# Performance work log

Measured on AMD Instinct MI355X. Metric: run time of the kernel, lower is better.

The kernel has to match this reference:

```python
import jax, jax.numpy as jnp
import numpy as np

DK, DL, HID = 128, 128, 128  # per init_kwargs: mlp_list=[256,128,128]


def setup_inputs() -> dict:
    key = jax.random.key(0)
    k1, k2, k3, k4, k5 = jax.random.split(key, 5)
    B, K, L = 2, 128, 4096
    inputA = jax.random.normal(k1, (B, K, DK), dtype=jnp.float32)
    inputB = jax.random.normal(k2, (B, L, DL), dtype=jnp.float32)
    # MLP layer 0: Linear(256 -> 128), kaiming-uniform-ish init
    lim1 = 1.0 / np.sqrt(DK + DL)
    W1 = jax.random.uniform(k3, (DK + DL, HID), jnp.float32, -lim1, lim1)
    b1 = jax.random.uniform(k4, (HID,), jnp.float32, -lim1, lim1)
    # scoring Linear(128 -> 1, bias=False)
    lim2 = 1.0 / np.sqrt(HID)
    w2 = jax.random.uniform(k5, (HID,), jnp.float32, -lim2, lim2)
    return {"inputA": inputA, "inputB": inputB, "W1": W1, "b1": b1,
            "w2": w2, "nA": K, "nB": L}


def reference(inputA, inputB, W1, b1, w2, nA, nB):
    # Original: tC = cat([repeat(A), repeat(B)], -1); mlp(tC); linear; softmax(L).
    # Fused-equivalent math: split W1 rows between the A-part and B-part of the
    # concat, so the first Linear is two small matmuls + broadcast add.
    hA = jnp.einsum('bkd,dh->bkh', inputA, W1[:DK])        # (B, K, H)
    hB = jnp.einsum('bld,dh->blh', inputB, W1[DK:])        # (B, L, H)
    h = jax.nn.relu(hA[:, :, None, :] + hB[:, None, :, :] + b1)  # (B, K, L, H)
    scores = jnp.einsum('bklh,h->bkl', h, w2)              # (B, K, L)
    return jax.nn.softmax(scores, axis=2)
```

## Files before the change

### kernel.cpp

```cpp
#include <hip/hip_runtime.h>
#include <hip/hip_fp16.h>
#include <math.h>

constexpr int BB = 2;
constexpr int KK = 128;
constexpr int LL = 4096;
constexpr int DD = 128;
constexpr int HH = 128;

__device__ __forceinline__ float4 ld4(const float* p) {
    return *reinterpret_cast<const float4*>(p);
}

__device__ __forceinline__ __half2 hmax2(__half2 a, __half2 b) {
    unsigned ua = __builtin_bit_cast(unsigned, a);
    unsigned ub = __builtin_bit_cast(unsigned, b);
    unsigned ud;
    asm("v_pk_max_f16 %0, %1, %2" : "=v"(ud) : "v"(ua), "v"(ub));
    return __builtin_bit_cast(__half2, ud);
}

__global__ __launch_bounds__(256) void k1_gemm(
    const float* __restrict__ inA, const float* __restrict__ inB,
    const float* __restrict__ W1, const float* __restrict__ b1,
    __half* __restrict__ uh, __half* __restrict__ vh)
{
    __shared__ __align__(16) float sIn[32 * 128];

    const int row0 = blockIdx.x * 32;
    const bool isA = (row0 < BB * KK);
    const float* src = isA ? (inA + (size_t)row0 * DD)
                           : (inB + (size_t)(row0 - BB * KK) * DD);
    const float* w   = W1 + (isA ? 0 : DD * HH);
    __half* dst      = isA ? (uh + (size_t)row0 * HH)
                           : (vh + (size_t)(row0 - BB * KK) * HH);

    const int tid = threadIdx.x;

    #pragma unroll
    for (int j = 0; j < 4; ++j) {
        const int idx = tid + 256 * j;
        reinterpret_cast<float4*>(sIn)[idx] =
            reinterpret_cast<const float4*>(src)[idx];
    }
    __syncthreads();

    const int tx = tid & 31;
    const int ty = tid >> 5;

    float accx[4], accy[4], accz[4], accw[4];
    #pragma unroll
    for (int r = 0; r < 4; ++r) { accx[r] = accy[r] = accz[r] = accw[r] = 0.f; }

    for (int d0 = 0; d0 < DD; d0 += 4) {
        float4 w4[4];
        #pragma unroll
        for (int dd = 0; dd < 4; ++dd)
            w4[dd] = ld4(&w[(size_t)(d0 + dd) * HH + tx * 4]);
        float a[4][4];
        #pragma unroll
        for (int r = 0; r < 4; ++r) {
            float4 a4 = ld4(&sIn[(ty * 4 + r) * 128 + d0]);
            a[r][0] = a4.x; a[r][1] = a4.y; a[r][2] = a4.z; a[r][3] = a4.w;
        }
        #pragma unroll
        for (int dd = 0; dd < 4; ++dd) {
            const float4 wv = w4[dd];
            #pragma unroll
            for (int r = 0; r < 4; ++r) {
                const float av = a[r][dd];
                accx[r] = fmaf(av, wv.x, accx[r]);
                accy[r] = fmaf(av, wv.y, accy[r]);
                accz[r] = fmaf(av, wv.z, accz[r]);
                accw[r] = fmaf(av, wv.w, accw[r]);
            }
        }
    }

    if (isA) {
        const float4 bb = ld4(&b1[tx * 4]);
        #pragma unroll
        for (int r = 0; r < 4; ++r) {
            accx[r] += bb.x; accy[r] += bb.y; accz[r] += bb.z; accw[r] += bb.w;
        }
    }

    #pragma unroll
    for (int r = 0; r < 4; ++r) {
        __half2 p0 = __floats2half2_rn(accx[r], accy[r]);
        __half2 p1 = __floats2half2_rn(accz[r], accw[r]);
        __half2* dp = reinterpret_cast<__half2*>(dst + (size_t)(ty * 4 + r) * HH + tx * 4);
        dp[0] = p0; dp[1] = p1;
    }
}

__global__ __launch_bounds__(256) void k2_score(
    const __half* __restrict__ uh, const __half* __restrict__ vh,
    const float* __restrict__ w2, float* __restrict__ out)
{
    __shared__ __align__(16) __half sU[4 * 128];
    __shared__ __align__(16) __half sW[128];

    int bi = blockIdx.x;
    const int kt = bi & 31;  bi >>= 5;
    const int lt = bi & 7;   bi >>= 3;
    const int b  = bi;
    const int tid = threadIdx.x;

    if (tid < 64) {
        reinterpret_cast<float4*>(sU)[tid] =
            reinterpret_cast<const float4*>(uh + ((size_t)b * KK + kt * 4) * HH)[tid];
    } else if (tid < 96) {
        const int i = tid - 64;
        float4 wf = ld4(&w2[i * 4]);
        __half2* wp = reinterpret_cast<__half2*>(sW);
        wp[i * 2]     = __floats2half2_rn(wf.x, wf.y);
        wp[i * 2 + 1] = __floats2half2_rn(wf.z, wf.w);
    }
    __syncthreads();

    const int l0 = lt * 512 + tid;
    const __half* v0p = vh + ((size_t)b * LL + l0) * HH;
    const __half* v1p = v0p + 256 * HH;

    float facc[4][2];
    #pragma unroll
    for (int k = 0; k < 4; ++k) { facc[k][0] = 0.f; facc[k][1] = 0.f; }

    const __half2 hz = __float2half2_rn(0.f);

    for (int fc = 0; fc < 8; ++fc) {
        __half2 acc[4][2];
        #pragma unroll
        for (int k = 0; k < 4; ++k) { acc[k][0] = hz; acc[k][1] = hz; }

        #pragma unroll
        for (int c = 0; c < 2; ++c) {
            const int hc = fc * 2 + c;
            float4 v0 = ld4(reinterpret_cast<const float*>(v0p + hc * 8));
            float4 v1 = ld4(reinterpret_cast<const float*>(v1p + hc * 8));
            float4 wc = ld4(reinterpret_cast<const float*>(sW + hc * 8));
            const __half2* w2h = reinterpret_cast<const __half2*>(&wc);
            const __half2* v0h = reinterpret_cast<const __half2*>(&v0);
            const __half2* v1h = reinterpret_cast<const __half2*>(&v1);
            #pragma unroll
            for (int k = 0; k < 4; ++k) {
                float4 uc = ld4(reinterpret_cast<const float*>(sU + k * 128 + hc * 8));
                const __half2* uh2 = reinterpret_cast<const __half2*>(&uc);
                #pragma unroll
                for (int j = 0; j < 4; ++j) {
                    __half2 s0 = __hadd2(uh2[j], v0h[j]);
                    __half2 s1 = __hadd2(uh2[j], v1h[j]);
                    acc[k][0] = __hfma2(hmax2(s0, hz), w2h[j], acc[k][0]);
                    acc[k][1] = __hfma2(hmax2(s1, hz), w2h[j], acc[k][1]);
                }
            }
        }
        #pragma unroll
        for (int k = 0; k < 4; ++k) {
            float2 f0 = __half22float2(acc[k][0]);
            float2 f1 = __half22float2(acc[k][1]);
            facc[k][0] += f0.x + f0.y;
            facc[k][1] += f1.x + f1.y;
        }
    }

    #pragma unroll
    for (int k = 0; k < 4; ++k) {
        out[((size_t)b * KK + kt * 4 + k) * LL + l0]       = facc[k][0];
        out[((size_t)b * KK + kt * 4 + k) * LL + l0 + 256] = facc[k][1];
    }
}

__global__ __launch_bounds__(256) void k3_softmax(float* __restrict__ out)
{
    __shared__ float redm[4];
    __shared__ float reds[4];

    const int row = blockIdx.x;
    float* p = out + (size_t)row * LL;
    const int tid = threadIdx.x;

    float4 x[4];
    #pragma unroll
    for (int j = 0; j < 4; ++j)
        x[j] = reinterpret_cast<const float4*>(p)[tid + 256 * j];

    float m = x[0].x;
    #pragma unroll
    for (int j = 0; j < 4; ++j)
        m = fmaxf(m, fmaxf(fmaxf(x[j].x, x[j].y), fmaxf(x[j].z, x[j].w)));
    #pragma unroll
    for (int off = 32; off > 0; off >>= 1)
        m = fmaxf(m, __shfl_xor(m, off, 64));

    const int lane = tid & 63, wv = tid >> 6;
    if (lane == 0) redm[wv] = m;
    __syncthreads();
    m = fmaxf(fmaxf(redm[0], redm[1]), fmaxf(redm[2], redm[3]));

    float s = 0.f;
    #pragma unroll
    for (int j = 0; j < 4; ++j) {
        x[j].x = expf(x[j].x - m); s += x[j].x;
        x[j].y = expf(x[j].y - m); s += x[j].y;
        x[j].z = expf(x[j].z - m); s += x[j].z;
        x[j].w = expf(x[j].w - m); s += x[j].w;
    }
    #pragma unroll
    for (int off = 32; off > 0; off >>= 1)
        s += __shfl_xor(s, off, 64);
    if (lane == 0) reds[wv] = s;
    __syncthreads();
    s = (reds[0] + reds[1]) + (reds[2] + reds[3]);

    const float inv = 1.0f / s;
    #pragma unroll
    for (int j = 0; j < 4; ++j) {
        x[j].x *= inv; x[j].y *= inv; x[j].z *= inv; x[j].w *= inv;
        reinterpret_cast<float4*>(p)[tid + 256 * j] = x[j];
    }
}

extern "C" void kernel_launch(void* const* d_in, const int* in_sizes, int n_in,
                              void* d_out, int out_size, void* d_ws, size_t ws_size,
                              hipStream_t stream)
{
    const float* inA = (const float*)d_in[0];
    const float* inB = (const float*)d_in[1];
    const float* W1  = (const float*)d_in[2];
    const float* b1  = (const float*)d_in[3];
    const float* w2  = (const float*)d_in[4];
    float* out = (float*)d_out;

    __half* uh = (__half*)d_ws;
    __half* vh = (__half*)((char*)d_ws + 64 * 1024);

    hipLaunchKernelGGL(k1_gemm, dim3(264), dim3(256), 0, stream,
                       inA, inB, W1, b1, uh, vh);
    hipLaunchKernelGGL(k2_score, dim3(512), dim3(256), 0, stream,
                       uh, vh, w2, out);
    hipLaunchKernelGGL(k3_softmax, dim3(BB * KK), dim3(256), 0, stream, out);
}
```

Measured before the change: 32.73 us.

## Transpose V to H-major layout and pack two L positions per half2 lane

The first kernel now writes V transposed to an H-by-L half layout through a padded shared-memory transpose. It writes U and w2 as duplicated half2 words. The scoring kernel then packs two adjacent L positions into each half2 instead of pairing H dimensions, so each thread reads coalesced 32-bit words across L and does a single final conversion per k. U and w2 are read straight from global memory (scalar, wave-uniform) rather than staged in LDS, which removes the block barrier but doubles U storage and adds a transpose step to the GEMM.

```diff
diff --git a/kernel.cpp b/kernel.cpp
--- a/kernel.cpp
+++ b/kernel.cpp
@@ -20,20 +20,27 @@
     return __builtin_bit_cast(__half2, ud);
 }
 
+__device__ __forceinline__ uint32_t duph(float x) {
+    __half h = __float2half(x);
+    unsigned short us = __builtin_bit_cast(unsigned short, h);
+    return (uint32_t)us * 0x10001u;
+}
+
 __global__ __launch_bounds__(256) void k1_gemm(
     const float* __restrict__ inA, const float* __restrict__ inB,
     const float* __restrict__ W1, const float* __restrict__ b1,
-    __half* __restrict__ uh, __half* __restrict__ vh)
+    const float* __restrict__ w2,
+    uint32_t* __restrict__ u_dup, uint32_t* __restrict__ w2_dup,
+    __half* __restrict__ vT)
 {
     __shared__ __align__(16) float sIn[32 * 128];
+    __shared__ float sT[128 * 33];
 
     const int row0 = blockIdx.x * 32;
     const bool isA = (row0 < BB * KK);
     const float* src = isA ? (inA + (size_t)row0 * DD)
                            : (inB + (size_t)(row0 - BB * KK) * DD);
     const float* w   = W1 + (isA ? 0 : DD * HH);
-    __half* dst      = isA ? (uh + (size_t)row0 * HH)
-                           : (vh + (size_t)(row0 - BB * KK) * HH);
 
     const int tid = threadIdx.x;
 
@@ -81,95 +88,100 @@
         const float4 bb = ld4(&b1[tx * 4]);
         #pragma unroll
         for (int r = 0; r < 4; ++r) {
-            accx[r] += bb.x; accy[r] += bb.y; accz[r] += bb.z; accw[r] += bb.w;
-        }
-    }
-
-    #pragma unroll
-    for (int r = 0; r < 4; ++r) {
-        __half2 p0 = __floats2half2_rn(accx[r], accy[r]);
-        __half2 p1 = __floats2half2_rn(accz[r], accw[r]);
-        __half2* dp = reinterpret_cast<__half2*>(dst + (size_t)(ty * 4 + r) * HH + tx * 4);
-        dp[0] = p0; dp[1] = p1;
+            uint4 o;
+            o.x = duph(accx[r] + bb.x);
+            o.y = duph(accy[r] + bb.y);
+            o.z = duph(accz[r] + bb.z);
+            o.w = duph(accw[r] + bb.w);
+            *reinterpret_cast<uint4*>(&u_dup[(size_t)(row0 + ty * 4 + r) * HH + tx * 4]) = o;
+        }
+        if (blockIdx.x == 0 && tid < HH) w2_dup[tid] = duph(w2[tid]);
+    } else {
+        #pragma unroll
+        for (int r = 0; r < 4; ++r) {
+            const int l = ty * 4 + r;
+            sT[(tx * 4 + 0) * 33 + l] = accx[r];
+            sT[(tx * 4 + 1) * 33 + l] = accy[r];
+            sT[(tx * 4 + 2) * 33 + l] = accz[r];
+            sT[(tx * 4 + 3) * 33 + l] = accw[r];
+        }
+        __syncthreads();
+        const int h    = tid >> 1;
+        const int half = tid & 1;
+        const int rowB = row0 - BB * KK;
+        const int bsel = rowB >> 12;
+        const int l0   = (rowB & 4095) + half * 16;
+        uint32_t o[8];
+        #pragma unroll
+        for (int i = 0; i < 8; ++i) {
+            const float lo = sT[h * 33 + half * 16 + 2 * i];
+            const float hi = sT[h * 33 + half * 16 + 2 * i + 1];
+            o[i] = __builtin_bit_cast(uint32_t, __floats2half2_rn(lo, hi));
+        }
+        uint32_t* dst = reinterpret_cast<uint32_t*>(vT) +
+                        ((size_t)(bsel * HH + h) * LL + l0) / 2;
+        uint4 s0; s0.x = o[0]; s0.y = o[1]; s0.z = o[2]; s0.w = o[3];
+        uint4 s1; s1.x = o[4]; s1.y = o[5]; s1.z = o[6]; s1.w = o[7];
+        *reinterpret_cast<uint4*>(dst)     = s0;
+        *reinterpret_cast<uint4*>(dst + 4) = s1;
     }
 }
 
 __global__ __launch_bounds__(256) void k2_score(
-    const __half* __restrict__ uh, const __half* __restrict__ vh,
-    const float* __restrict__ w2, float* __restrict__ out)
-{
-    __shared__ __align__(16) __half sU[4 * 128];
-    __shared__ __align__(16) __half sW[128];
-
+    const uint32_t* __restrict__ u_dup, const uint32_t* __restrict__ w2_dup,
+    const __half* __restrict__ vT, float* __restrict__ out)
+{
     int bi = blockIdx.x;
     const int kt = bi & 31;  bi >>= 5;
     const int lt = bi & 7;   bi >>= 3;
     const int b  = bi;
     const int tid = threadIdx.x;
 
-    if (tid < 64) {
-        reinterpret_cast<float4*>(sU)[tid] =
-            reinterpret_cast<const float4*>(uh + ((size_t)b * KK + kt * 4) * HH)[tid];
-    } else if (tid < 96) {
-        const int i = tid - 64;
-        float4 wf = ld4(&w2[i * 4]);
-        __half2* wp = reinterpret_cast<__half2*>(sW);
-        wp[i * 2]     = __floats2half2_rn(wf.x, wf.y);
-        wp[i * 2 + 1] = __floats2half2_rn(wf.z, wf.w);
-    }
-    __syncthreads();
-
-    const int l0 = lt * 512 + tid;
-    const __half* v0p = vh + ((size_t)b * LL + l0) * HH;
-    const __half* v1p = v0p + 256 * HH;
-
-    float facc[4][2];
-    #pragma unroll
-    for (int k = 0; k < 4; ++k) { facc[k][0] = 0.f; facc[k][1] = 0.f; }
+    const int lp = lt * 256 + tid;
+    const uint32_t* vp = reinterpret_cast<const uint32_t*>(vT)
+                         + (size_t)b * HH * (LL / 2) + lp;
+    const uint32_t* up = u_dup + (size_t)(b * KK + kt * 4) * HH;
+
+    float2 facc[4];
+    #pragma unroll
+    for (int k = 0; k < 4; ++k) { facc[k].x = 0.f; facc[k].y = 0.f; }
 
     const __half2 hz = __float2half2_rn(0.f);
 
-    for (int fc = 0; fc < 8; ++fc) {
-        __half2 acc[4][2];
-        #pragma unroll
-        for (int k = 0; k < 4; ++k) { acc[k][0] = hz; acc[k][1] = hz; }
+    for (int g = 0; g < 8; ++g) {
+        __half2 acc[4];
+        #pragma unroll
+        for (int k = 0; k < 4; ++k) acc[k] = hz;
 
         #pragma unroll
         for (int c = 0; c < 2; ++c) {
-            const int hc = fc * 2 + c;
-            float4 v0 = ld4(reinterpret_cast<const float*>(v0p + hc * 8));
-            float4 v1 = ld4(reinterpret_cast<const float*>(v1p + hc * 8));
-            float4 wc = ld4(reinterpret_cast<const float*>(sW + hc * 8));
-            const __half2* w2h = reinterpret_cast<const __half2*>(&wc);
-            const __half2* v0h = reinterpret_cast<const __half2*>(&v0);
-            const __half2* v1h = reinterpret_cast<const __half2*>(&v1);
+            const int h0 = g * 16 + c * 8;
+            uint32_t v[8];
+            #pragma unroll
+            for (int j = 0; j < 8; ++j)
+                v[j] = vp[(size_t)(h0 + j) * (LL / 2)];
             #pragma unroll
             for (int k = 0; k < 4; ++k) {
-                float4 uc = ld4(reinterpret_cast<const float*>(sU + k * 128 + hc * 8));
-                const __half2* uh2 = reinterpret_cast<const __half2*>(&uc);
                 #pragma unroll
-                for (int j = 0; j < 4; ++j) {
-                    __half2 s0 = __hadd2(uh2[j], v0h[j]);
-                    __half2 s1 = __hadd2(uh2[j], v1h[j]);
-                    acc[k][0] = __hfma2(hmax2(s0, hz), w2h[j], acc[k][0]);
-                    acc[k][1] = __hfma2(hmax2(s1, hz), w2h[j], acc[k][1]);
+                for (int j = 0; j < 8; ++j) {
+                    const __half2 uu = __builtin_bit_cast(__half2, up[k * HH + h0 + j]);
+                    const __half2 ww = __builtin_bit_cast(__half2, w2_dup[h0 + j]);
+                    __half2 t = __hadd2(__builtin_bit_cast(__half2, v[j]), uu);
+                    acc[k] = __hfma2(hmax2(t, hz), ww, acc[k]);
                 }
             }
         }
         #pragma unroll
         for (int k = 0; k < 4; ++k) {
-            float2 f0 = __half22float2(acc[k][0]);
-            float2 f1 = __half22float2(acc[k][1]);
-            facc[k][0] += f0.x + f0.y;
-            facc[k][1] += f1.x + f1.y;
-        }
-    }
-
-    #pragma unroll
-    for (int k = 0; k < 4; ++k) {
-        out[((size_t)b * KK + kt * 4 + k) * LL + l0]       = facc[k][0];
-        out[((size_t)b * KK + kt * 4 + k) * LL + l0 + 256] = facc[k][1];
-    }
+            const float2 f = __half22float2(acc[k]);
+            facc[k].x += f.x; facc[k].y += f.y;
+        }
+    }
+
+    #pragma unroll
+    for (int k = 0; k < 4; ++k)
+        *reinterpret_cast<float2*>(
+            &out[(size_t)(b * KK + kt * 4 + k) * LL + 2 * lp]) = facc[k];
 }
 
 __global__ __launch_bounds__(256) void k3_softmax(float* __restrict__ out)
@@ -233,12 +245,13 @@
     const float* w2  = (const float*)d_in[4];
     float* out = (float*)d_out;
 
-    __half* uh = (__half*)d_ws;
-    __half* vh = (__half*)((char*)d_ws + 64 * 1024);
+    uint32_t* u_dup  = (uint32_t*)d_ws;
+    uint32_t* w2_dup = (uint32_t*)((char*)d_ws + 128 * 1024);
+    __half*   vT     = (__half*)((char*)d_ws + 128 * 1024 + 512);
 
     hipLaunchKernelGGL(k1_gemm, dim3(264), dim3(256), 0, stream,
-                       inA, inB, W1, b1, uh, vh);
+                       inA, inB, W1, b1, w2, u_dup, w2_dup, vT);
     hipLaunchKernelGGL(k2_score, dim3(512), dim3(256), 0, stream,
-                       uh, vh, w2, out);
+                       u_dup, w2_dup, vT, out);
     hipLaunchKernelGGL(k3_softmax, dim3(BB * KK), dim3(256), 0, stream, out);
 }
```

After: 33.01 us. No clear change (+0.9%).
